# Optimization experiments

Measured on AMD Instinct MI355X. Metric: run time of the kernel, lower is better.

## Reference

```python
import jax, jax.numpy as jnp
import numpy as np

N, E, EMB, HID, H = 50000, 800000, 128, 512, 8
D = EMB // H
EPS = 1e-5


def _linear_params(key, fan_in, fan_out):
    s = 1.0 / np.sqrt(fan_in)
    k1, k2 = jax.random.split(key)
    w = jax.random.uniform(k1, (fan_in, fan_out), minval=-s, maxval=s, dtype=jnp.float32)
    b = jax.random.uniform(k2, (fan_out,), minval=-s, maxval=s, dtype=jnp.float32)
    return w, b


def setup_inputs() -> dict:
    key = jax.random.key(0)
    ks = jax.random.split(key, 9)
    x = jax.random.normal(ks[0], (N, EMB), dtype=jnp.float32)
    edge_index = jax.random.randint(ks[1], (2, E), 0, N, dtype=jnp.int32)
    batch = jnp.zeros((N,), dtype=jnp.int32)
    wq, bq = _linear_params(ks[2], EMB, EMB)
    wk, bk = _linear_params(ks[3], EMB, EMB)
    wv, bv = _linear_params(ks[4], EMB, EMB)
    wo, bo = _linear_params(ks[5], EMB, EMB)
    w1, b1 = _linear_params(ks[6], EMB, HID)
    w2, b2 = _linear_params(ks[7], HID, EMB)
    g1 = jnp.ones((EMB,), jnp.float32); be1 = jnp.zeros((EMB,), jnp.float32)
    g2 = jnp.ones((EMB,), jnp.float32); be2 = jnp.zeros((EMB,), jnp.float32)
    return {"x": x, "wq": wq, "bq": bq, "wk": wk, "bk": bk, "wv": wv, "bv": bv,
            "wo": wo, "bo": bo, "w1": w1, "b1": b1, "w2": w2, "b2": b2,
            "g1": g1, "be1": be1, "g2": g2, "be2": be2,
            "edge_index": edge_index, "batch": batch, "latent": 0}


def _batchnorm(x, g, b):
    mu = x.mean(axis=0)
    var = ((x - mu) ** 2).mean(axis=0)  # biased, as BatchNorm1d in training
    return g * (x - mu) * jax.lax.rsqrt(var + EPS) + b


def _forward(x, wq, bq, wk, bk, wv, bv, wo, bo, w1, b1, w2, b2, g1, be1, g2, be2, A, B):
    n = x.shape[0]
    q = (x @ wq + bq).reshape(n, H, D)
    k = (x @ wk + bk).reshape(n, H, D)
    v = (x @ wv + bv).reshape(n, H, D)
    # per-edge head-mixing scores: q[A] @ k[B]^T -> [E, H, H]
    score = jnp.einsum('ehd,egd->ehg', q[A], k[B])
    ssum = jax.ops.segment_sum(score, A, num_segments=n)
    cnt = jax.ops.segment_sum(jnp.ones((A.shape[0],), score.dtype), A, num_segments=n)
    score = ssum / jnp.maximum(cnt, 1.0)[:, None, None]  # scatter-mean per node [N,H,H]
    score = jax.nn.softmax(score, axis=-1)
    out = jnp.einsum('ehg,egd->ehd', score, v).reshape(n, EMB)
    out = out @ wo + bo
    x = _batchnorm(out + x, g1, be1)
    h = jax.nn.gelu(x @ w1 + b1, approximate=False)
    h = h @ w2 + b2
    x = _batchnorm(h + x, g2, be2)
    return x


def reference(x, wq, bq, wk, bk, wv, bv, wo, bo, w1, b1, w2, b2, g1, be1, g2, be2, edge_index, batch, latent):
    A, B = edge_index[0], edge_index[1]
    return _forward(x, wq, bq, wk, bk, wv, bv, wo, bo, w1, b1, w2, b2, g1, be1, g2, be2, A, B)
```

## Files before the change

### kernel.cpp

```cpp
#include <hip/hip_runtime.h>
#include <hip/hip_bf16.h>

typedef float f4 __attribute__((ext_vector_type(4)));
typedef short bh8 __attribute__((ext_vector_type(8)));

#define EMB 128
#define HID 512

__device__ __forceinline__ float bfbits2f(unsigned int lo16) {
    unsigned int u = lo16 << 16;
    return __builtin_bit_cast(float, u);
}
__device__ __forceinline__ short f2bf(float f) {
    __hip_bfloat16 h = __float2bfloat16(f);
    return __builtin_bit_cast(short, h);
}
__device__ __forceinline__ float gelu_fast(float x) {
    float x3 = x * x * x;
    float y = 1.5957691216f * x + 0.0713548163f * x3;
    return x / (1.0f + __expf(-y));
}

__global__ void hist_kernel(const int* __restrict__ edge, unsigned* __restrict__ cnt, int E) {
    int stride = gridDim.x * blockDim.x;
    for (int e = blockIdx.x * blockDim.x + threadIdx.x; e < E; e += stride)
        atomicAdd(&cnt[edge[e]], 1u);
}

__global__ void scan_blocks(const unsigned* __restrict__ cnt, int* __restrict__ off,
                            int* __restrict__ bsum, int n) {
    __shared__ int ls[256];
    int tid = threadIdx.x;
    int base = blockIdx.x * 1024 + tid * 4;
    int v0 = 0, v1 = 0, v2 = 0, v3 = 0;
    if (base + 0 < n) v0 = (int)cnt[base + 0];
    if (base + 1 < n) v1 = (int)cnt[base + 1];
    if (base + 2 < n) v2 = (int)cnt[base + 2];
    if (base + 3 < n) v3 = (int)cnt[base + 3];
    int s = v0 + v1 + v2 + v3;
    ls[tid] = s;
    __syncthreads();
    for (int d = 1; d < 256; d <<= 1) {
        int t = (tid >= d) ? ls[tid - d] : 0;
        __syncthreads();
        ls[tid] += t;
        __syncthreads();
    }
    int incl = ls[tid];
    int run = incl - s;
    if (tid == 255) bsum[blockIdx.x] = incl;
    if (base + 0 < n) { off[base + 0] = run; run += v0; }
    if (base + 1 < n) { off[base + 1] = run; run += v1; }
    if (base + 2 < n) { off[base + 2] = run; run += v2; }
    if (base + 3 < n) { off[base + 3] = run; }
}

__global__ void scan_bsums(int* __restrict__ bsum, int nb) {
    int lane = threadIdx.x & 63;
    int x = (lane < nb) ? bsum[lane] : 0;
    int orig = x;
#pragma unroll
    for (int o = 1; o < 64; o <<= 1) {
        int t = __shfl_up(x, o, 64);
        if (lane >= o) x += t;
    }
    if (lane < nb) bsum[lane] = x - orig;
}

__global__ void scan_apply(const unsigned* __restrict__ cnt, const int* __restrict__ bsum,
                           int* __restrict__ off, int* __restrict__ offw,
                           float* __restrict__ cntf, int n) {
    int base = blockIdx.x * 1024 + threadIdx.x * 4;
    int add = bsum[blockIdx.x];
#pragma unroll
    for (int i = 0; i < 4; ++i) {
        int idx = base + i;
        if (idx < n) {
            int o = off[idx] + add;
            off[idx] = o;
            offw[idx] = o;
            cntf[idx] = (float)cnt[idx];
        }
    }
}

__global__ void place_kernel(const int* __restrict__ edge, int* __restrict__ offw,
                             int* __restrict__ sortedB, int E) {
    int stride = gridDim.x * blockDim.x;
    for (int e = blockIdx.x * blockDim.x + threadIdx.x; e < E; e += stride) {
        int a = edge[e];
        int pos = atomicAdd(&offw[a], 1);
        sortedB[pos] = edge[E + e];
    }
}

__global__ void prep_all(const float* __restrict__ wq, const float* __restrict__ wk,
                         const float* __restrict__ wv, const float* __restrict__ wo,
                         const float* __restrict__ w1, const float* __restrict__ w2,
                         const float* __restrict__ bq, const float* __restrict__ bk,
                         const float* __restrict__ bv,
                         short* __restrict__ wqkvT, short* __restrict__ woT,
                         short* __restrict__ w1T, short* __restrict__ w2T,
                         float* __restrict__ bqkv) {
    int id = blockIdx.x * blockDim.x + threadIdx.x;
    if (id < 16384) {
        int k = id >> 7, c = id & 127;
        wqkvT[c * 128 + k] = f2bf(wq[id]);
    } else if (id < 32768) {
        int t = id - 16384; int k = t >> 7, c = t & 127;
        wqkvT[(128 + c) * 128 + k] = f2bf(wk[t]);
    } else if (id < 49152) {
        int t = id - 32768; int k = t >> 7, c = t & 127;
        wqkvT[(256 + c) * 128 + k] = f2bf(wv[t]);
    } else if (id < 65536) {
        int t = id - 49152; int k = t >> 7, c = t & 127;
        woT[c * 128 + k] = f2bf(wo[t]);
    } else if (id < 131072) {
        int t = id - 65536; int k = t >> 9, c = t & 511;
        w1T[c * 128 + k] = f2bf(w1[t]);
    } else if (id < 196608) {
        int t = id - 131072; int k = t >> 7, c = t & 127;
        w2T[c * 512 + k] = f2bf(w2[t]);
    }
    if (id < 128) {
        bqkv[id] = bq[id];
        bqkv[128 + id] = bk[id];
        bqkv[256 + id] = bv[id];
    }
}

template<int KT, bool IN_BF16>
__device__ __forceinline__ void ld_ab(bh8 (&av)[4], bh8 (&bv)[4],
                                      const float* __restrict__ Xf, const short* __restrict__ Xb,
                                      const int (&rowA)[4], const short* __restrict__ Wt,
                                      int C0, int l15, int kbase) {
#pragma unroll
    for (int rf = 0; rf < 4; ++rf) {
        if constexpr (IN_BF16) {
            av[rf] = *(const bh8*)(Xb + (size_t)rowA[rf] * KT + kbase);
        } else {
            f4 lo = *(const f4*)(Xf + (size_t)rowA[rf] * KT + kbase);
            f4 hi = *(const f4*)(Xf + (size_t)rowA[rf] * KT + kbase + 4);
            bh8 t;
            t[0] = f2bf(lo[0]); t[1] = f2bf(lo[1]); t[2] = f2bf(lo[2]); t[3] = f2bf(lo[3]);
            t[4] = f2bf(hi[0]); t[5] = f2bf(hi[1]); t[6] = f2bf(hi[2]); t[7] = f2bf(hi[3]);
            av[rf] = t;
        }
    }
#pragma unroll
    for (int cf = 0; cf < 4; ++cf)
        bv[cf] = *(const bh8*)(Wt + (size_t)(C0 + cf * 16 + l15) * KT + kbase);
}

__device__ __forceinline__ void mm16(f4 (&acc)[4][4], const bh8 (&av)[4], const bh8 (&bv)[4]) {
#pragma unroll
    for (int rf = 0; rf < 4; ++rf)
#pragma unroll
        for (int cf = 0; cf < 4; ++cf)
            acc[rf][cf] = __builtin_amdgcn_mfma_f32_16x16x32_bf16(av[rf], bv[cf], acc[rf][cf], 0, 0, 0);
}

#define CSTRIDE 136

template<int KT, bool IN_BF16, bool GELU, bool OUT_BF16, bool RESID, bool RBF16, bool STATS>
__global__ __launch_bounds__(256, 2) void mfma_gemm(
    const void* __restrict__ Xv, const short* __restrict__ Wt, const float* __restrict__ bias,
    const void* __restrict__ resid,
    void* __restrict__ outv, float* __restrict__ slots, int n, int OC, int ncolb, int nrb)
{
    int bx, by;
    if (ncolb == 1) {
        bx = blockIdx.x; by = 0;
    } else {
        int q = blockIdx.x >> 3;
        by = q % ncolb;
        bx = (q / ncolb) * 8 + (blockIdx.x & 7);
        if (bx >= nrb) return;
    }
    const int lane = threadIdx.x & 63;
    const int w = threadIdx.x >> 6;
    const int wr = w >> 1, wc = w & 1;
    const int R0 = bx * 128 + wr * 64;
    const int C0 = by * 128 + wc * 64;
    const int l15 = lane & 15;
    const int kg = lane >> 4;

    const float* Xf = (const float*)Xv;
    const short* Xb = (const short*)Xv;

    int rowA[4];
#pragma unroll
    for (int rf = 0; rf < 4; ++rf) rowA[rf] = min(R0 + rf * 16 + l15, n - 1);

    f4 acc[4][4];
#pragma unroll
    for (int rf = 0; rf < 4; ++rf)
#pragma unroll
        for (int cf = 0; cf < 4; ++cf) acc[rf][cf] = 0.f;

    constexpr int NT = KT / 32;
    bh8 aA[4], bA[4], aB[4], bB[4];

    ld_ab<KT, IN_BF16>(aA, bA, Xf, Xb, rowA, Wt, C0, l15, kg * 8);
#pragma unroll
    for (int t = 0; t < NT; t += 2) {
        ld_ab<KT, IN_BF16>(aB, bB, Xf, Xb, rowA, Wt, C0, l15, (t + 1) * 32 + kg * 8);
        mm16(acc, aA, bA);
        if (t + 2 < NT)
            ld_ab<KT, IN_BF16>(aA, bA, Xf, Xb, rowA, Wt, C0, l15, (t + 2) * 32 + kg * 8);
        mm16(acc, aB, bB);
    }

    if constexpr (OUT_BF16) {
        extern __shared__ short cs[];
        const int lrb = wr * 64;
        const int lcb = wc * 64;
#pragma unroll
        for (int cf = 0; cf < 4; ++cf) {
            const float bcol = bias[C0 + cf * 16 + l15];
#pragma unroll
            for (int rf = 0; rf < 4; ++rf) {
#pragma unroll
                for (int i = 0; i < 4; ++i) {
                    float val = acc[rf][cf][i] + bcol;
                    if constexpr (GELU) val = gelu_fast(val);
                    cs[(lrb + rf * 16 + kg * 4 + i) * CSTRIDE + lcb + cf * 16 + l15] = f2bf(val);
                }
            }
        }
        __syncthreads();
        const int tc = threadIdx.x & 15;
        const int tr = threadIdx.x >> 4;
        const int gcb = by * 128;
#pragma unroll
        for (int r = 0; r < 8; ++r) {
            int lrow = tr + r * 16;
            int grow = bx * 128 + lrow;
            if (grow < n) {
                bh8 v = *(bh8*)(cs + lrow * CSTRIDE + tc * 8);
                *(bh8*)((short*)outv + (size_t)grow * OC + gcb + tc * 8) = v;
            }
        }
    } else {
#pragma unroll
        for (int cf = 0; cf < 4; ++cf) {
            const int col = C0 + cf * 16 + l15;
            const float bcol = bias[col];
#pragma unroll
            for (int rf = 0; rf < 4; ++rf) {
                float s = 0.f, q = 0.f;
#pragma unroll
                for (int i = 0; i < 4; ++i) {
                    const int row = R0 + rf * 16 + kg * 4 + i;
                    if (row < n) {
                        float val = acc[rf][cf][i] + bcol;
                        if constexpr (RESID) {
                            float rv;
                            if constexpr (RBF16)
                                rv = bfbits2f((unsigned short)((const short*)resid)[(size_t)row * EMB + col]);
                            else
                                rv = ((const float*)resid)[(size_t)row * EMB + col];
                            val += rv;
                        }
                        if constexpr (GELU) val = gelu_fast(val);
                        if constexpr (STATS) { s += val; q += val * val; }
                        ((float*)outv)[(size_t)row * OC + col] = val;
                    }
                }
                if constexpr (STATS) {
                    s += __shfl_xor(s, 16, 64); s += __shfl_xor(s, 32, 64);
                    q += __shfl_xor(q, 16, 64); q += __shfl_xor(q, 32, 64);
                    if (kg == 0) {
                        float* sl = slots + (size_t)(bx & 63) * 256;
                        unsafeAtomicAdd(&sl[col], s);
                        unsafeAtomicAdd(&sl[128 + col], q);
                    }
                }
            }
        }
    }
}

__global__ __launch_bounds__(256, 2) void ffn_fused(
    const short* __restrict__ xn1, const short* __restrict__ w1T, const float* __restrict__ b1,
    const short* __restrict__ w2T, const float* __restrict__ b2,
    float* __restrict__ y2, float* __restrict__ slots, int n)
{
    extern __shared__ short hs[];
    const int bx = blockIdx.x;
    const int lane = threadIdx.x & 63;
    const int w = threadIdx.x >> 6;
    const int wr = w >> 1, wc = w & 1;
    const int R0 = bx * 128 + wr * 64;
    const int l15 = lane & 15;
    const int kg = lane >> 4;

    int rowA[4];
#pragma unroll
    for (int rf = 0; rf < 4; ++rf) rowA[rf] = min(R0 + rf * 16 + l15, n - 1);

    bh8 aF0[4], aF1[4], aF2[4], aF3[4];
#pragma unroll
    for (int rf = 0; rf < 4; ++rf) {
        const short* p = xn1 + (size_t)rowA[rf] * EMB + kg * 8;
        aF0[rf] = *(const bh8*)(p);
        aF1[rf] = *(const bh8*)(p + 32);
        aF2[rf] = *(const bh8*)(p + 64);
        aF3[rf] = *(const bh8*)(p + 96);
    }

    f4 acc2[4][4];
#pragma unroll
    for (int rf = 0; rf < 4; ++rf)
#pragma unroll
        for (int cf = 0; cf < 4; ++cf) acc2[rf][cf] = 0.f;

    const int lrb = wr * 64;
    const int lcb = wc * 64;

    for (int c = 0; c < 4; ++c) {
        f4 acc1[4][4];
#pragma unroll
        for (int rf = 0; rf < 4; ++rf)
#pragma unroll
            for (int cf = 0; cf < 4; ++cf) acc1[rf][cf] = 0.f;

        bh8 bP[4], bQ[4];
        auto ldB1 = [&](bh8 (&dst)[4], int ks) {
#pragma unroll
            for (int cf = 0; cf < 4; ++cf) {
                int col = c * 128 + wc * 64 + cf * 16 + l15;
                dst[cf] = *(const bh8*)(w1T + (size_t)col * EMB + ks * 32 + kg * 8);
            }
        };
        ldB1(bP, 0);
        ldB1(bQ, 1);
        mm16(acc1, aF0, bP);
        ldB1(bP, 2);
        mm16(acc1, aF1, bQ);
        ldB1(bQ, 3);
        mm16(acc1, aF2, bP);
        mm16(acc1, aF3, bQ);

        __syncthreads();
#pragma unroll
        for (int cf = 0; cf < 4; ++cf) {
            const float bcol = b1[c * 128 + wc * 64 + cf * 16 + l15];
#pragma unroll
            for (int rf = 0; rf < 4; ++rf) {
#pragma unroll
                for (int i = 0; i < 4; ++i) {
                    float val = gelu_fast(acc1[rf][cf][i] + bcol);
                    hs[(lrb + rf * 16 + kg * 4 + i) * CSTRIDE + lcb + cf * 16 + l15] = f2bf(val);
                }
            }
        }
        __syncthreads();

        bh8 aP[4], aQ[4];
        auto ldA2 = [&](bh8 (&dst)[4], int ks) {
#pragma unroll
            for (int rf = 0; rf < 4; ++rf)
                dst[rf] = *(const bh8*)(hs + (wr * 64 + rf * 16 + l15) * CSTRIDE + ks * 32 + kg * 8);
        };
        auto ldB2 = [&](bh8 (&dst)[4], int ks) {
#pragma unroll
            for (int cf = 0; cf < 4; ++cf) {
                int col = wc * 64 + cf * 16 + l15;
                dst[cf] = *(const bh8*)(w2T + (size_t)col * HID + c * 128 + ks * 32 + kg * 8);
            }
        };
        ldA2(aP, 0); ldB2(bP, 0);
        ldA2(aQ, 1); ldB2(bQ, 1);
        mm16(acc2, aP, bP);
        ldA2(aP, 2); ldB2(bP, 2);
        mm16(acc2, aQ, bQ);
        ldA2(aQ, 3); ldB2(bQ, 3);
        mm16(acc2, aP, bP);
        mm16(acc2, aQ, bQ);
    }

    const int C0 = wc * 64;
#pragma unroll
    for (int cf = 0; cf < 4; ++cf) {
        const int col = C0 + cf * 16 + l15;
        const float bcol = b2[col];
#pragma unroll
        for (int rf = 0; rf < 4; ++rf) {
            float s = 0.f, q = 0.f;
#pragma unroll
            for (int i = 0; i < 4; ++i) {
                const int row = R0 + rf * 16 + kg * 4 + i;
                if (row < n) {
                    float val = acc2[rf][cf][i] + bcol;
                    val += bfbits2f((unsigned short)xn1[(size_t)row * EMB + col]);
                    s += val; q += val * val;
                    y2[(size_t)row * EMB + col] = val;
                }
            }
            s += __shfl_xor(s, 16, 64); s += __shfl_xor(s, 32, 64);
            q += __shfl_xor(q, 16, 64); q += __shfl_xor(q, 32, 64);
            if (kg == 0) {
                float* sl = slots + (size_t)(bx & 63) * 256;
                unsafeAtomicAdd(&sl[col], s);
                unsafeAtomicAdd(&sl[128 + col], q);
            }
        }
    }
}

__global__ void gather_attn_kernel(const short* __restrict__ qkv, const int* __restrict__ off,
                                   const unsigned* __restrict__ cnt, const int* __restrict__ sortedB,
                                   const float* __restrict__ cntf, short* __restrict__ attno, int n) {
    int wid = (int)((blockIdx.x * blockDim.x + threadIdx.x) >> 6);
    int lane = threadIdx.x & 63;
    int nw = (gridDim.x * blockDim.x) >> 6;
    const int l15 = lane & 15;
    const int grp = lane >> 4;
    const int h = lane >> 3, g = lane & 7;
    for (int node = wid; node < n; node += nw) {
        int start = off[node];
        int deg = (int)cnt[node];
        float a[8];
#pragma unroll
        for (int i = 0; i < 8; ++i) a[i] = 0.f;
        for (int j = 0; j < deg; j += 8) {
            int i0 = j + grp, i1 = j + 4 + grp;
            uint4 u0 = make_uint4(0, 0, 0, 0), u1 = make_uint4(0, 0, 0, 0);
            if (i0 < deg) {
                int b = sortedB[start + i0];
                u0 = *(const uint4*)(qkv + (size_t)b * 384 + 128 + l15 * 8);
            }
            if (i1 < deg) {
                int b = sortedB[start + i1];
                u1 = *(const uint4*)(qkv + (size_t)b * 384 + 128 + l15 * 8);
            }
            unsigned w0[4] = {u0.x, u0.y, u0.z, u0.w};
            unsigned w1[4] = {u1.x, u1.y, u1.z, u1.w};
#pragma unroll
            for (int i = 0; i < 4; ++i) {
                a[2 * i]     += bfbits2f(w0[i] & 0xffffu) + bfbits2f(w1[i] & 0xffffu);
                a[2 * i + 1] += bfbits2f(w0[i] >> 16)     + bfbits2f(w1[i] >> 16);
            }
        }
#pragma unroll
        for (int i = 0; i < 8; ++i) {
            a[i] += __shfl_xor(a[i], 16, 64);
            a[i] += __shfl_xor(a[i], 32, 64);
        }

        const short* qp = qkv + (size_t)node * 384 + h * 16;
        uint4 qa = *(const uint4*)qp;
        uint4 qb = *(const uint4*)(qp + 8);
        float qv[16];
        {
            unsigned ua[4] = {qa.x, qa.y, qa.z, qa.w};
            unsigned ub[4] = {qb.x, qb.y, qb.z, qb.w};
#pragma unroll
            for (int w2 = 0; w2 < 4; ++w2) {
                qv[2 * w2]         = bfbits2f(ua[w2] & 0xffffu);
                qv[2 * w2 + 1]     = bfbits2f(ua[w2] >> 16);
                qv[8 + 2 * w2]     = bfbits2f(ub[w2] & 0xffffu);
                qv[8 + 2 * w2 + 1] = bfbits2f(ub[w2] >> 16);
            }
        }
        float s = 0.f;
#pragma unroll
        for (int i = 0; i < 8; ++i) {
            s += qv[i]     * __shfl(a[i], 2 * g, 64);
            s += qv[8 + i] * __shfl(a[i], 2 * g + 1, 64);
        }
        float c = cntf[node];
        s *= 1.0f / fmaxf(c, 1.0f);
        float m = s;
#pragma unroll
        for (int o = 1; o < 8; o <<= 1) m = fmaxf(m, __shfl_xor(m, o, 64));
        float e = __expf(s - m);
        float sum = e;
#pragma unroll
        for (int o = 1; o < 8; o <<= 1) sum += __shfl_xor(sum, o, 64);
        float p = e / sum;
        float o0 = 0.f, o1 = 0.f;
        int d0 = g * 2;
#pragma unroll
        for (int gg = 0; gg < 8; ++gg) {
            float pg = __shfl(p, h * 8 + gg, 64);
            unsigned vv = *(const unsigned*)(qkv + (size_t)node * 384 + 256 + gg * 16 + d0);
            o0 += pg * bfbits2f(vv & 0xffffu);
            o1 += pg * bfbits2f(vv >> 16);
        }
        unsigned pk = (unsigned)(unsigned short)f2bf(o0) | ((unsigned)(unsigned short)f2bf(o1) << 16);
        *(unsigned*)(attno + (size_t)node * EMB + h * 16 + d0) = pk;
    }
}

__global__ void bn_finalize_slots(const float* __restrict__ slots, float* __restrict__ scsh,
                                  const float* __restrict__ g, const float* __restrict__ be, int n) {
    int c = threadIdx.x;
    float s = 0.f, q = 0.f;
    for (int i = 0; i < 64; ++i) {
        s += slots[(size_t)i * 256 + c];
        q += slots[(size_t)i * 256 + 128 + c];
    }
    float invn = 1.0f / (float)n;
    float mean = s * invn;
    float var = fmaxf(q * invn - mean * mean, 0.f);
    float sc = g[c] * rsqrtf(var + 1e-5f);
    scsh[c] = sc;
    scsh[128 + c] = be[c] - mean * sc;
}

__global__ void apply_bn_bf16(const float* __restrict__ Y, const float* __restrict__ scsh,
                              short* __restrict__ out, size_t total8) {
    size_t stride = (size_t)gridDim.x * blockDim.x;
    for (size_t i = (size_t)blockIdx.x * blockDim.x + threadIdx.x; i < total8; i += stride) {
        size_t base = i * 8;
        f4 lo = *(const f4*)(Y + base);
        f4 hi = *(const f4*)(Y + base + 4);
        int c = (int)(base & 127);
        f4 s0 = *(const f4*)(scsh + c);
        f4 s1 = *(const f4*)(scsh + c + 4);
        f4 h0 = *(const f4*)(scsh + 128 + c);
        f4 h1 = *(const f4*)(scsh + 128 + c + 4);
        lo = lo * s0 + h0;
        hi = hi * s1 + h1;
        bh8 o;
        o[0] = f2bf(lo[0]); o[1] = f2bf(lo[1]); o[2] = f2bf(lo[2]); o[3] = f2bf(lo[3]);
        o[4] = f2bf(hi[0]); o[5] = f2bf(hi[1]); o[6] = f2bf(hi[2]); o[7] = f2bf(hi[3]);
        *(bh8*)(out + base) = o;
    }
}

__global__ void bn_apply(float* __restrict__ Y, const float* __restrict__ scsh, size_t total4) {
    size_t stride = (size_t)gridDim.x * blockDim.x;
    for (size_t i = (size_t)blockIdx.x * blockDim.x + threadIdx.x; i < total4; i += stride) {
        f4 vv = ((f4*)Y)[i];
        int c = (int)((i * 4) & 127);
#pragma unroll
        for (int j = 0; j < 4; ++j) vv[j] = vv[j] * scsh[c + j] + scsh[128 + c + j];
        ((f4*)Y)[i] = vv;
    }
}

extern "C" void kernel_launch(void* const* d_in, const int* in_sizes, int n_in,
                              void* d_out, int out_size, void* d_ws, size_t ws_size,
                              hipStream_t stream) {
    const float* x   = (const float*)d_in[0];
    const float* wq  = (const float*)d_in[1];
    const float* bq  = (const float*)d_in[2];
    const float* wk  = (const float*)d_in[3];
    const float* bk  = (const float*)d_in[4];
    const float* wv  = (const float*)d_in[5];
    const float* bv  = (const float*)d_in[6];
    const float* wo  = (const float*)d_in[7];
    const float* bo  = (const float*)d_in[8];
    const float* w1  = (const float*)d_in[9];
    const float* b1  = (const float*)d_in[10];
    const float* w2  = (const float*)d_in[11];
    const float* b2  = (const float*)d_in[12];
    const float* g1  = (const float*)d_in[13];
    const float* be1 = (const float*)d_in[14];
    const float* g2  = (const float*)d_in[15];
    const float* be2 = (const float*)d_in[16];
    const int* edge  = (const int*)d_in[17];

    int n = in_sizes[0] / EMB;
    int E = in_sizes[17] / 2;

    float* wsf = (float*)d_ws;
    unsigned* cnt_u = (unsigned*)wsf;
    float*  cntf  = wsf + 65536;
    int*    off   = (int*)(wsf + 2 * 65536);
    int*    offw  = (int*)(wsf + 3 * 65536);
    int*    bsum  = (int*)(wsf + 4 * 65536);
    int*    sortedB = (int*)(wsf + 4 * 65536 + 64);
    float*  base5 = wsf + 4 * 65536 + 64 + E;
    short*  qkv   = (short*)base5;
    short*  attno = (short*)(base5 + (size_t)n * 256);
    float*  y1    = base5 + (size_t)n * 320;
    float*  warea = y1 + (size_t)n * 128;
    short*  wqkvT = (short*)warea;
    short*  woT   = wqkvT + 384 * 128;
    short*  w1T   = woT + 128 * 128;
    short*  w2T   = w1T + 512 * 128;
    float*  bqkv  = (float*)(w2T + 128 * 512);
    float*  slots1 = bqkv + 384;
    float*  slots2 = slots1 + 64 * 256;
    float*  scsh1  = slots2 + 64 * 256;
    float*  scsh2  = scsh1 + 256;
    short*  xn1   = attno;
    float*  y2    = (float*)d_out;

    hipMemsetAsync(cnt_u, 0, 65536 * sizeof(unsigned), stream);
    hipMemsetAsync(slots1, 0, 2 * 64 * 256 * sizeof(float), stream);

    int nb = (n + 1023) / 1024;
    hist_kernel<<<2048, 256, 0, stream>>>(edge, cnt_u, E);
    scan_blocks<<<nb, 256, 0, stream>>>(cnt_u, off, bsum, n);
    scan_bsums<<<1, 64, 0, stream>>>(bsum, nb);
    scan_apply<<<nb, 256, 0, stream>>>(cnt_u, bsum, off, offw, cntf, n);
    place_kernel<<<2048, 256, 0, stream>>>(edge, offw, sortedB, E);

    prep_all<<<768, 256, 0, stream>>>(wq, wk, wv, wo, w1, w2, bq, bk, bv,
                                      wqkvT, woT, w1T, w2T, bqkv);

    int nrb = (n + 127) / 128;
    int nrb8 = ((nrb + 7) / 8) * 8;
    const size_t CSH = 128 * CSTRIDE * sizeof(short);

    mfma_gemm<128, false, false, true, false, false, false><<<nrb8 * 3, 256, CSH, stream>>>(
        x, wqkvT, bqkv, nullptr, qkv, nullptr, n, 384, 3, nrb);

    gather_attn_kernel<<<6144, 256, 0, stream>>>(qkv, off, cnt_u, sortedB, cntf, attno, n);

    mfma_gemm<128, true, false, false, true, false, true><<<nrb, 256, 0, stream>>>(
        attno, woT, bo, x, y1, slots1, n, EMB, 1, nrb);

    bn_finalize_slots<<<1, 128, 0, stream>>>(slots1, scsh1, g1, be1, n);

    apply_bn_bf16<<<1600, 256, 0, stream>>>(y1, scsh1, xn1, (size_t)n * EMB / 8);

    ffn_fused<<<nrb, 256, CSH, stream>>>(xn1, w1T, b1, w2T, b2, y2, slots2, n);

    bn_finalize_slots<<<1, 128, 0, stream>>>(slots2, scsh2, g2, be2, n);
    bn_apply<<<512, 256, 0, stream>>>(y2, scsh2, (size_t)n * EMB / 4);
}
```

Baseline: 300.9 us.

## Fuse edge placement into QKV GEMM launch and fold BN1 apply into FFN

The edge-placement scatter (atomic slot claim plus sortedB write) now runs in extra blocks appended to the QKV GEMM grid, so it overlaps with the GEMM instead of being a separate serial launch. Separately, the standalone BN1 apply kernel that wrote a bf16 normalized copy is removed, and ffn_fused instead reads the fp32 y1, applies scale/shift and converts to bf16 in registers, including for the residual. This saves a kernel launch and a full write and read of the intermediate, at the cost of reading fp32 (twice the bytes) inside the FFN and extra ALU work there. The residual now uses unrounded fp32 normalized values, which changes numerics slightly.

After: 287.9 us. 1.05x faster.

```diff
diff --git a/kernel.cpp b/kernel.cpp
--- a/kernel.cpp
+++ b/kernel.cpp
@@ -81,16 +81,6 @@
             offw[idx] = o;
             cntf[idx] = (float)cnt[idx];
         }
-    }
-}
-
-__global__ void place_kernel(const int* __restrict__ edge, int* __restrict__ offw,
-                             int* __restrict__ sortedB, int E) {
-    int stride = gridDim.x * blockDim.x;
-    for (int e = blockIdx.x * blockDim.x + threadIdx.x; e < E; e += stride) {
-        int a = edge[e];
-        int pos = atomicAdd(&offw[a], 1);
-        sortedB[pos] = edge[E + e];
     }
 }
 
@@ -162,12 +152,26 @@
 
 #define CSTRIDE 136
 
-template<int KT, bool IN_BF16, bool GELU, bool OUT_BF16, bool RESID, bool RBF16, bool STATS>
+template<int KT, bool IN_BF16, bool GELU, bool OUT_BF16, bool RESID, bool RBF16, bool STATS, bool PLACE>
 __global__ __launch_bounds__(256, 2) void mfma_gemm(
     const void* __restrict__ Xv, const short* __restrict__ Wt, const float* __restrict__ bias,
     const void* __restrict__ resid,
-    void* __restrict__ outv, float* __restrict__ slots, int n, int OC, int ncolb, int nrb)
+    void* __restrict__ outv, float* __restrict__ slots, int n, int OC, int ncolb, int nrb,
+    const int* __restrict__ edge, int* __restrict__ offw, int* __restrict__ sortedB,
+    int E, int gemmBlocks)
 {
+    if constexpr (PLACE) {
+        if ((int)blockIdx.x >= gemmBlocks) {
+            int tid0 = (blockIdx.x - gemmBlocks) * 256 + threadIdx.x;
+            int stride = (gridDim.x - gemmBlocks) * 256;
+            for (int e = tid0; e < E; e += stride) {
+                int a = edge[e];
+                int pos = atomicAdd(&offw[a], 1);
+                sortedB[pos] = edge[E + e];
+            }
+            return;
+        }
+    }
     int bx, by;
     if (ncolb == 1) {
         bx = blockIdx.x; by = 0;
@@ -282,7 +286,8 @@
 }
 
 __global__ __launch_bounds__(256, 2) void ffn_fused(
-    const short* __restrict__ xn1, const short* __restrict__ w1T, const float* __restrict__ b1,
+    const float* __restrict__ y1, const float* __restrict__ scsh1,
+    const short* __restrict__ w1T, const float* __restrict__ b1,
     const short* __restrict__ w2T, const float* __restrict__ b2,
     float* __restrict__ y2, float* __restrict__ slots, int n)
 {
@@ -301,12 +306,27 @@
 
     bh8 aF0[4], aF1[4], aF2[4], aF3[4];
 #pragma unroll
-    for (int rf = 0; rf < 4; ++rf) {
-        const short* p = xn1 + (size_t)rowA[rf] * EMB + kg * 8;
-        aF0[rf] = *(const bh8*)(p);
-        aF1[rf] = *(const bh8*)(p + 32);
-        aF2[rf] = *(const bh8*)(p + 64);
-        aF3[rf] = *(const bh8*)(p + 96);
+    for (int seg = 0; seg < 4; ++seg) {
+        const int kb = seg * 32 + kg * 8;
+        f4 s0 = *(const f4*)(scsh1 + kb);
+        f4 s1 = *(const f4*)(scsh1 + kb + 4);
+        f4 h0 = *(const f4*)(scsh1 + 128 + kb);
+        f4 h1 = *(const f4*)(scsh1 + 128 + kb + 4);
+#pragma unroll
+        for (int rf = 0; rf < 4; ++rf) {
+            const float* p = y1 + (size_t)rowA[rf] * EMB + kb;
+            f4 lo = *(const f4*)(p);
+            f4 hi = *(const f4*)(p + 4);
+            lo = lo * s0 + h0;
+            hi = hi * s1 + h1;
+            bh8 t;
+            t[0] = f2bf(lo[0]); t[1] = f2bf(lo[1]); t[2] = f2bf(lo[2]); t[3] = f2bf(lo[3]);
+            t[4] = f2bf(hi[0]); t[5] = f2bf(hi[1]); t[6] = f2bf(hi[2]); t[7] = f2bf(hi[3]);
+            if (seg == 0) aF0[rf] = t;
+            else if (seg == 1) aF1[rf] = t;
+            else if (seg == 2) aF2[rf] = t;
+            else aF3[rf] = t;
+        }
     }
 
     f4 acc2[4][4];
@@ -385,6 +405,8 @@
     for (int cf = 0; cf < 4; ++cf) {
         const int col = C0 + cf * 16 + l15;
         const float bcol = b2[col];
+        const float scv = scsh1[col];
+        const float shv = scsh1[128 + col];
 #pragma unroll
         for (int rf = 0; rf < 4; ++rf) {
             float s = 0.f, q = 0.f;
@@ -393,7 +415,7 @@
                 const int row = R0 + rf * 16 + kg * 4 + i;
                 if (row < n) {
                     float val = acc2[rf][cf][i] + bcol;
-                    val += bfbits2f((unsigned short)xn1[(size_t)row * EMB + col]);
+                    val += y1[(size_t)row * EMB + col] * scv + shv;
                     s += val; q += val * val;
                     y2[(size_t)row * EMB + col] = val;
                 }
@@ -508,27 +530,6 @@
     float sc = g[c] * rsqrtf(var + 1e-5f);
     scsh[c] = sc;
     scsh[128 + c] = be[c] - mean * sc;
-}
-
-__global__ void apply_bn_bf16(const float* __restrict__ Y, const float* __restrict__ scsh,
-                              short* __restrict__ out, size_t total8) {
-    size_t stride = (size_t)gridDim.x * blockDim.x;
-    for (size_t i = (size_t)blockIdx.x * blockDim.x + threadIdx.x; i < total8; i += stride) {
-        size_t base = i * 8;
-        f4 lo = *(const f4*)(Y + base);
-        f4 hi = *(const f4*)(Y + base + 4);
-        int c = (int)(base & 127);
-        f4 s0 = *(const f4*)(scsh + c);
-        f4 s1 = *(const f4*)(scsh + c + 4);
-        f4 h0 = *(const f4*)(scsh + 128 + c);
-        f4 h1 = *(const f4*)(scsh + 128 + c + 4);
-        lo = lo * s0 + h0;
-        hi = hi * s1 + h1;
-        bh8 o;
-        o[0] = f2bf(lo[0]); o[1] = f2bf(lo[1]); o[2] = f2bf(lo[2]); o[3] = f2bf(lo[3]);
-        o[4] = f2bf(hi[0]); o[5] = f2bf(hi[1]); o[6] = f2bf(hi[2]); o[7] = f2bf(hi[3]);
-        *(bh8*)(out + base) = o;
-    }
 }
 
 __global__ void bn_apply(float* __restrict__ Y, const float* __restrict__ scsh, size_t total4) {
@@ -588,7 +589,6 @@
     float*  slots2 = slots1 + 64 * 256;
     float*  scsh1  = slots2 + 64 * 256;
     float*  scsh2  = scsh1 + 256;
-    short*  xn1   = attno;
     float*  y2    = (float*)d_out;
 
     hipMemsetAsync(cnt_u, 0, 65536 * sizeof(unsigned), stream);
@@ -599,7 +599,6 @@
     scan_blocks<<<nb, 256, 0, stream>>>(cnt_u, off, bsum, n);
     scan_bsums<<<1, 64, 0, stream>>>(bsum, nb);
     scan_apply<<<nb, 256, 0, stream>>>(cnt_u, bsum, off, offw, cntf, n);
-    place_kernel<<<2048, 256, 0, stream>>>(edge, offw, sortedB, E);
 
     prep_all<<<768, 256, 0, stream>>>(wq, wk, wv, wo, w1, w2, bq, bk, bv,
                                       wqkvT, woT, w1T, w2T, bqkv);
@@ -607,20 +606,22 @@
     int nrb = (n + 127) / 128;
     int nrb8 = ((nrb + 7) / 8) * 8;
     const size_t CSH = 128 * CSTRIDE * sizeof(short);
-
-    mfma_gemm<128, false, false, true, false, false, false><<<nrb8 * 3, 256, CSH, stream>>>(
-        x, wqkvT, bqkv, nullptr, qkv, nullptr, n, 384, 3, nrb);
+    const int PLACE_BLK = 1024;
+
+    mfma_gemm<128, false, false, true, false, false, false, true>
+        <<<nrb8 * 3 + PLACE_BLK, 256, CSH, stream>>>(
+        x, wqkvT, bqkv, nullptr, qkv, nullptr, n, 384, 3, nrb,
+        edge, offw, sortedB, E, nrb8 * 3);
 
     gather_attn_kernel<<<6144, 256, 0, stream>>>(qkv, off, cnt_u, sortedB, cntf, attno, n);
 
-    mfma_gemm<128, true, false, false, true, false, true><<<nrb, 256, 0, stream>>>(
-        attno, woT, bo, x, y1, slots1, n, EMB, 1, nrb);
+    mfma_gemm<128, true, false, false, true, false, true, false><<<nrb, 256, 0, stream>>>(
+        attno, woT, bo, x, y1, slots1, n, EMB, 1, nrb,
+        nullptr, nullptr, nullptr, 0, 0);
 
     bn_finalize_slots<<<1, 128, 0, stream>>>(slots1, scsh1, g1, be1, n);
 
-    apply_bn_bf16<<<1600, 256, 0, stream>>>(y1, scsh1, xn1, (size_t)n * EMB / 8);
-
-    ffn_fused<<<nrb, 256, CSH, stream>>>(xn1, w1T, b1, w2T, b2, y2, slots2, n);
+    ffn_fused<<<nrb, 256, CSH, stream>>>(y1, scsh1, w1T, b1, w2T, b2, y2, slots2, n);
 
     bn_finalize_slots<<<1, 128, 0, stream>>>(slots2, scsh2, g2, be2, n);
     bn_apply<<<512, 256, 0, stream>>>(y2, scsh2, (size_t)n * EMB / 4);
```
